# Optimization experiments

Measured on AMD Instinct MI355X. Metric: run time of the kernel, lower is better.

Reference implementation:

```python
import jax, jax.numpy as jnp
import numpy as np

GAMMA = 1.0
MAX_SIMILARITY = 1.0


def setup_inputs() -> dict:
    key = jax.random.key(0)
    k1, k2 = jax.random.split(key)
    B, Ns, D = 128, 512, 256
    d_vectors = jax.random.normal(k1, (B, Ns, D), dtype=jnp.float32)
    # Normalized similarity matrix (MinMaxScaler output lies in [0, 1])
    S = jax.random.uniform(k2, (Ns, Ns), dtype=jnp.float32)
    return {"d_vectors": d_vectors, "S": S}


def reference(d_vectors, S):
    B, Ns, D = d_vectors.shape
    eye = jnp.eye(Ns, dtype=d_vectors.dtype)

    # Pairwise squared distances: ||di||^2 + ||dj||^2 - 2 di.dj  -> [B, Ns, Ns]
    n2 = jnp.sum(d_vectors * d_vectors, axis=-1)  # [B, Ns]
    sq = n2[:, :, None] + n2[:, None, :] - 2.0 * jnp.einsum("bid,bjd->bij", d_vectors, d_vectors)
    sq = jnp.maximum(sq, 0.0) * (1.0 - eye)  # exact zero on the diagonal

    # Safe sqrt (subgradient 0 at zero distance, matching torch.norm)
    dist = jnp.where(sq > 0, jnp.sqrt(jnp.where(sq > 0, sq, 1.0)), 0.0)
    Kd = jnp.exp(-GAMMA * dist)  # Gaussian-kernel Gram matrix [B, Ns, Ns]

    # Norm-ratio loss
    W = (S > 0).astype(d_vectors.dtype)  # [Ns, Ns]
    denom = jnp.linalg.norm(W - eye)  # Frobenius norm, scalar
    Kd_tilde = Kd * (1.0 - eye)  # zero diagonal
    S_tilde = S - MAX_SIMILARITY * eye
    diff = W * (Kd_tilde - S_tilde)  # broadcast over batch
    numer = jnp.sqrt(jnp.sum(diff * diff, axis=(1, 2)))  # [B]
    losses = 2.0 * numer / denom
    return jnp.sum(losses)
```

## Files before the change

kernel.cpp:

```cpp
#include <hip/hip_runtime.h>
#include <hip/hip_bf16.h>

typedef __bf16 bf16_t;
typedef __bf16 bf16x4 __attribute__((ext_vector_type(4)));
typedef __bf16 bf16x8 __attribute__((ext_vector_type(8)));
typedef float f32x4 __attribute__((ext_vector_type(4)));
typedef float f32x16 __attribute__((ext_vector_type(16)));
typedef long i64x2 __attribute__((ext_vector_type(2)));
typedef int i32x4 __attribute__((ext_vector_type(4)));

#define BATCH 128
#define NS 512
#define DIM 256
#define BT 128
#define NT 10
#define LDSP 272

__global__ __launch_bounds__(256) void prep_st_kernel(const float* __restrict__ dv,
                                                      const float* __restrict__ S,
                                                      unsigned char* __restrict__ f8,
                                                      float* __restrict__ n2g,
                                                      float* __restrict__ St,
                                                      float* __restrict__ dpartial) {
    const int bidx = blockIdx.x;
    const int t = threadIdx.x;
    if (bidx < 256) {
        const int bi = bidx >> 4, bj = bidx & 15;
        const int c  = t & 31, r0 = t >> 5;
        __shared__ float tileS[32][33];
        __shared__ float red[4];
        float dacc = 0.0f;
#pragma unroll
        for (int k = 0; k < 4; ++k) {
            const int r  = r0 + k * 8;
            const int gi = bi * 32 + r, gj = bj * 32 + c;
            const float s = S[(size_t)gi * NS + gj];
            tileS[r][c] = s;
            const float w = (s > 0.0f) ? 1.0f : 0.0f;
            const float e = (gi == gj) ? 1.0f : 0.0f;
            const float d = w - e;
            dacc += d * d;
        }
        __syncthreads();
#pragma unroll
        for (int k = 0; k < 4; ++k) {
            const int r = r0 + k * 8;
            St[(size_t)(bj * 32 + r) * NS + bi * 32 + c] = tileS[c][r];
        }
        const int lane = t & 63, wave = t >> 6;
#pragma unroll
        for (int off = 32; off >= 1; off >>= 1) dacc += __shfl_down(dacc, off, 64);
        if (lane == 0) red[wave] = dacc;
        __syncthreads();
        if (t == 0) dpartial[bidx] = red[0] + red[1] + red[2] + red[3];
    } else {
        const int wid  = ((bidx - 256) << 2) | (t >> 6);
        const int lane = t & 63;
#pragma unroll
        for (int it = 0; it < 8; ++it) {
            const int row = wid + it * 8192;
            const f32x4 v = *reinterpret_cast<const f32x4*>(dv + (size_t)row * DIM + lane * 4);
            float pn = v[0]*v[0] + v[1]*v[1] + v[2]*v[2] + v[3]*v[3];
#pragma unroll
            for (int off = 32; off >= 1; off >>= 1) pn += __shfl_xor(pn, off, 64);
            int w0 = __builtin_amdgcn_cvt_pk_fp8_f32(v[0], v[1], 0, false);
            w0     = __builtin_amdgcn_cvt_pk_fp8_f32(v[2], v[3], w0, true);
            *reinterpret_cast<int*>(f8 + (size_t)row * DIM + lane * 4) = w0;
            if (lane == 0) n2g[row] = pn;
        }
    }
}

__global__ __launch_bounds__(512, 4) void gram_pair_kernel(const unsigned char* __restrict__ f8,
                                                           const float* __restrict__ n2g,
                                                           const float* __restrict__ S,
                                                           const float* __restrict__ St,
                                                           float* __restrict__ partial) {
    const int bid  = blockIdx.x;
    const int work = (bid & 7) * 160 + (bid >> 3);
    const int b    = work / NT;
    const int idx  = work - b * NT;
    int ti, tj;
    if (idx < 4)      { ti = 0; tj = idx; }
    else if (idx < 7) { ti = 1; tj = idx - 3; }
    else if (idx < 9) { ti = 2; tj = idx - 5; }
    else              { ti = 3; tj = 3; }
    const bool diag = (ti == tj);
    const int t    = threadIdx.x;
    const int wave = t >> 6, lane = t & 63;
    const int wr   = wave >> 2, wc = wave & 3;
    const int col  = lane & 31, kh = lane >> 5;

    __shared__ char  sP[256 * LDSP];
    __shared__ float n2s[256];
    __shared__ float red[8];

    {
        const int g     = t >> 8;
        const int tg    = t & 255;
        const int off16 = (tg & 15) * 16;
        const int rbase = tg >> 4;
        if (g == 0 || !diag) {
            const int psel = g ? tj : ti;
            const unsigned char* src = f8 + ((size_t)b * NS + (size_t)psel * BT) * DIM;
#pragma unroll
            for (int it = 0; it < 8; ++it) {
                const int row = it * 16 + rbase;
                const i32x4 v = *reinterpret_cast<const i32x4*>(src + (size_t)row * DIM + off16);
                *reinterpret_cast<i32x4*>(&sP[(g * 128 + row) * LDSP + off16]) = v;
            }
        }
        if (t < 256) {
            const int p = t >> 7;
            if (p == 0 || !diag) {
                const int psel2 = p ? tj : ti;
                n2s[t] = n2g[(size_t)b * NS + (size_t)psel2 * BT + (t & 127)];
            }
        }
    }
    __syncthreads();

    const int boff = diag ? 0 : 128;
    const char* aP = &sP[(wr * 64 + col) * LDSP + kh * 16];
    const char* bP = &sP[(boff + wc * 32 + col) * LDSP + kh * 16];
    f32x16 acc0 = (f32x16)(0.0f);
    f32x16 acc1 = (f32x16)(0.0f);
    __builtin_amdgcn_s_setprio(1);
#pragma unroll
    for (int u = 0; u < 8; ++u) {
        const i64x2 A0 = *reinterpret_cast<const i64x2*>(aP + u * 32);
        const i64x2 A1 = *reinterpret_cast<const i64x2*>(aP + 32 * LDSP + u * 32);
        const i64x2 Bv = *reinterpret_cast<const i64x2*>(bP + u * 32);
        acc0 = __builtin_amdgcn_mfma_f32_32x32x16_fp8_fp8(A0[0], Bv[0], acc0, 0, 0, 0);
        acc1 = __builtin_amdgcn_mfma_f32_32x32x16_fp8_fp8(A1[0], Bv[0], acc1, 0, 0, 0);
        acc0 = __builtin_amdgcn_mfma_f32_32x32x16_fp8_fp8(A0[1], Bv[1], acc0, 0, 0, 0);
        acc1 = __builtin_amdgcn_mfma_f32_32x32x16_fp8_fp8(A1[1], Bv[1], acc1, 0, 0, 0);
    }
    __builtin_amdgcn_s_setprio(0);

    float local = 0.0f;
    {
        const int lj = wc * 32 + col;
        const int gj = tj * BT + lj;
        const float n2j = n2s[boff + lj];
        const float* Strow = St + (size_t)gj * NS + ti * BT;
        const float* Srow  = S  + (size_t)gj * NS + ti * BT;
#pragma unroll
        for (int m = 0; m < 2; ++m) {
            const f32x16 av = m ? acc1 : acc0;
#pragma unroll
            for (int h4 = 0; h4 < 4; ++h4) {
                const int li0 = wr * 64 + m * 32 + h4 * 8 + kh * 4;
                const f32x4 s1v = *reinterpret_cast<const f32x4*>(Strow + li0);
                f32x4 s2v = (f32x4)(0.0f);
                if (!diag) s2v = *reinterpret_cast<const f32x4*>(Srow + li0);
#pragma unroll
                for (int e = 0; e < 4; ++e) {
                    const int li = li0 + e;
                    const float c = av[h4 * 4 + e];
                    const float sq = fmaxf(n2s[li] + n2j - 2.0f * c, 0.0f);
                    const float dist = __builtin_amdgcn_sqrtf(sq);
                    const float kd = __expf(-dist);
                    const float s1 = s1v[e];
                    if (diag) {
                        float d = (li == lj) ? (1.0f - s1) : (kd - s1);
                        d *= (s1 > 0.0f) ? 1.0f : 0.0f;
                        local += d * d;
                    } else {
                        const float s2 = s2v[e];
                        const float d1 = (s1 > 0.0f) ? (kd - s1) : 0.0f;
                        const float d2 = (s2 > 0.0f) ? (kd - s2) : 0.0f;
                        local += d1 * d1 + d2 * d2;
                    }
                }
            }
        }
    }

#pragma unroll
    for (int off = 32; off >= 1; off >>= 1) local += __shfl_down(local, off, 64);
    if (lane == 0) red[wave] = local;
    __syncthreads();
    if (t == 0) {
        float s = 0.0f;
#pragma unroll
        for (int w = 0; w < 8; ++w) s += red[w];
        partial[(size_t)b * NT + idx] = s;
    }
}


__global__ __launch_bounds__(256) void norms_kernel(const float* __restrict__ dv,
                                                    float* __restrict__ n2) {
    const int row  = blockIdx.x * 4 + (threadIdx.x >> 6);
    const int lane = threadIdx.x & 63;
    const float4 v = *reinterpret_cast<const float4*>(dv + (size_t)row * DIM + lane * 4);
    float s = v.x * v.x + v.y * v.y + v.z * v.z + v.w * v.w;
#pragma unroll
    for (int off = 32; off >= 1; off >>= 1) s += __shfl_down(s, off, 64);
    if (lane == 0) n2[row] = s;
}

__global__ __launch_bounds__(256) void denom_kernel(const float* __restrict__ Smat,
                                                    float* __restrict__ dpartial) {
    const int t = threadIdx.x;
    const int lane = t & 63, wave = t >> 6;
    __shared__ float sred[4];
    float acc = 0.0f;
    const int base = blockIdx.x * 512;
#pragma unroll
    for (int r = 0; r < 2; ++r) {
        const int v4 = base + r * 256 + t;
        const float4 s4 = reinterpret_cast<const float4*>(Smat)[v4];
        const int idx0 = v4 * 4;
        const int i = idx0 >> 9;
#pragma unroll
        for (int c = 0; c < 4; ++c) {
            const float s = (&s4.x)[c];
            const int j = (idx0 + c) & (NS - 1);
            const float w = (s > 0.0f) ? 1.0f : 0.0f;
            const float e = (i == j) ? 1.0f : 0.0f;
            const float d = w - e;
            acc += d * d;
        }
    }
#pragma unroll
    for (int off = 32; off >= 1; off >>= 1) acc += __shfl_down(acc, off, 64);
    if (lane == 0) sred[wave] = acc;
    __syncthreads();
    if (t == 0) dpartial[blockIdx.x] = sred[0] + sred[1] + sred[2] + sred[3];
}

#define FLDSK 40
__global__ __launch_bounds__(256) void gram_f32_kernel(const float* __restrict__ dv,
                                                       const float* __restrict__ Smat,
                                                       const float* __restrict__ n2,
                                                       float* __restrict__ partial) {
    const int tile = blockIdx.x;
    const int b    = blockIdx.y;
    const int ti   = tile >> 2, tj = tile & 3;
    const int t    = threadIdx.x;
    const int wave = t >> 6, lane = t & 63;
    const int wr   = wave >> 1, wc = wave & 1;

    __shared__ bf16_t sA[BT * FLDSK];
    __shared__ bf16_t sB[BT * FLDSK];
    __shared__ float red[4];

    const float* Abase = dv + ((size_t)b * NS + (size_t)ti * BT) * DIM;
    const float* Bbase = dv + ((size_t)b * NS + (size_t)tj * BT) * DIM;

    f32x4 acc[4][4];
#pragma unroll
    for (int m = 0; m < 4; ++m)
#pragma unroll
        for (int n = 0; n < 4; ++n) acc[m][n] = (f32x4)(0.0f);

    const int fr = lane & 15;
    const int g  = lane >> 4;

    for (int ks = 0; ks < DIM; ks += 32) {
        float4 ra[4], rb[4];
#pragma unroll
        for (int i = 0; i < 4; ++i) {
            const int c   = i * 256 + t;
            const int row = c >> 3;
            const int kc  = (c & 7) * 4;
            ra[i] = *reinterpret_cast<const float4*>(Abase + (size_t)row * DIM + ks + kc);
            rb[i] = *reinterpret_cast<const float4*>(Bbase + (size_t)row * DIM + ks + kc);
        }
        __syncthreads();
#pragma unroll
        for (int i = 0; i < 4; ++i) {
            const int c   = i * 256 + t;
            const int row = c >> 3;
            const int kc  = (c & 7) * 4;
            bf16x4 va = { (bf16_t)ra[i].x, (bf16_t)ra[i].y, (bf16_t)ra[i].z, (bf16_t)ra[i].w };
            bf16x4 vb = { (bf16_t)rb[i].x, (bf16_t)rb[i].y, (bf16_t)rb[i].z, (bf16_t)rb[i].w };
            *reinterpret_cast<bf16x4*>(&sA[row * FLDSK + kc]) = va;
            *reinterpret_cast<bf16x4*>(&sB[row * FLDSK + kc]) = vb;
        }
        __syncthreads();

        bf16x8 afrag[4], bfrag[4];
#pragma unroll
        for (int m = 0; m < 4; ++m)
            afrag[m] = *reinterpret_cast<const bf16x8*>(&sA[(wr * 64 + m * 16 + fr) * FLDSK + g * 8]);
#pragma unroll
        for (int n = 0; n < 4; ++n)
            bfrag[n] = *reinterpret_cast<const bf16x8*>(&sB[(wc * 64 + n * 16 + fr) * FLDSK + g * 8]);
#pragma unroll
        for (int m = 0; m < 4; ++m)
#pragma unroll
            for (int n = 0; n < 4; ++n)
                acc[m][n] = __builtin_amdgcn_mfma_f32_16x16x32_bf16(afrag[m], bfrag[n], acc[m][n], 0, 0, 0);
    }

    float local = 0.0f;
    const float* n2b = n2 + (size_t)b * NS;
    const int rowbase = ti * BT + wr * 64;
    const int colbase = tj * BT + wc * 64;
#pragma unroll
    for (int m = 0; m < 4; ++m) {
#pragma unroll
        for (int n = 0; n < 4; ++n) {
            const int gi0 = rowbase + m * 16 + g * 4;
            const int gj  = colbase + n * 16 + fr;
            const float ncol = n2b[gj];
#pragma unroll
            for (int j = 0; j < 4; ++j) {
                const int gi = gi0 + j;
                const float cij = acc[m][n][j];
                float sq = fmaxf(n2b[gi] + ncol - 2.0f * cij, 0.0f);
                const float dist = sqrtf(sq);
                const float kd = __expf(-dist);
                const float s = Smat[(size_t)gi * NS + gj];
                const float w = (s > 0.0f) ? 1.0f : 0.0f;
                float d = (gi == gj) ? (1.0f - s) : (kd - s);
                d *= w;
                local += d * d;
            }
        }
    }
#pragma unroll
    for (int off = 32; off >= 1; off >>= 1) local += __shfl_down(local, off, 64);
    if (lane == 0) red[wave] = local;
    __syncthreads();
    if (t == 0) partial[(size_t)b * 16 + tile] = red[0] + red[1] + red[2] + red[3];
}

__global__ __launch_bounds__(256) void finalize_kernel(const float* __restrict__ dpartial, int ndp,
                                                       const float* __restrict__ partial, int ntiles,
                                                       float* __restrict__ out) {
    const int t = threadIdx.x;
    const int lane = t & 63, wave = t >> 6;
    __shared__ float sred[4];
    __shared__ float sred2[4];

    float dacc = (t < ndp) ? dpartial[t] : 0.0f;
#pragma unroll
    for (int off = 32; off >= 1; off >>= 1) dacc += __shfl_down(dacc, off, 64);
    if (lane == 0) sred[wave] = dacc;
    __syncthreads();
    const float denom = sqrtf(sred[0] + sred[1] + sred[2] + sred[3]);

    float lsum = 0.0f;
    if (t < BATCH) {
        float ss = 0.0f;
        for (int k = 0; k < ntiles; ++k) ss += partial[(size_t)t * ntiles + k];
        lsum = 2.0f * sqrtf(ss) / denom;
    }
#pragma unroll
    for (int off = 32; off >= 1; off >>= 1) lsum += __shfl_down(lsum, off, 64);
    if (lane == 0) sred2[wave] = lsum;
    __syncthreads();
    if (t == 0) out[0] = sred2[0] + sred2[1] + sred2[2] + sred2[3];
}

extern "C" void kernel_launch(void* const* d_in, const int* in_sizes, int n_in,
                              void* d_out, int out_size, void* d_ws, size_t ws_size,
                              hipStream_t stream) {
    const float* dv   = (const float*)d_in[0];
    const float* Smat = (const float*)d_in[1];
    float* out = (float*)d_out;

    const size_t f8_bytes = (size_t)BATCH * NS * DIM;
    const size_t st_bytes = (size_t)NS * NS * 4;
    const size_t n2_bytes = (size_t)BATCH * NS * 4;
    const size_t pt_bytes = (size_t)BATCH * 16 * 4;
    const size_t dp_bytes = 256 * 4;
    const size_t need = f8_bytes + st_bytes + n2_bytes + pt_bytes + dp_bytes;

    if (ws_size >= need) {
        char* w = (char*)d_ws;
        unsigned char* f8 = (unsigned char*)w;  w += f8_bytes;
        float* St      = (float*)w;   w += st_bytes;
        float* n2g     = (float*)w;   w += n2_bytes;
        float* partial = (float*)w;   w += pt_bytes;
        float* dpart   = (float*)w;

        prep_st_kernel<<<dim3(2304), 256, 0, stream>>>(dv, Smat, f8, n2g, St, dpart);
        gram_pair_kernel<<<dim3(NT * BATCH), 512, 0, stream>>>(f8, n2g, Smat, St, partial);
        finalize_kernel<<<dim3(1), 256, 0, stream>>>(dpart, 256, partial, NT, out);
    } else {
        float* n2      = (float*)d_ws;
        float* partial = n2 + (size_t)BATCH * NS;
        float* dpart   = partial + (size_t)BATCH * 16;

        norms_kernel<<<dim3(BATCH * NS / 4), 256, 0, stream>>>(dv, n2);
        denom_kernel<<<dim3(128), 256, 0, stream>>>(Smat, dpart);
        gram_f32_kernel<<<dim3(16, BATCH), 256, 0, stream>>>(dv, Smat, n2, partial);
        finalize_kernel<<<dim3(1), 256, 0, stream>>>(dpart, 128, partial, 16, out);
    }
}
```

Baseline: 51.90 us.

## Stage Gram kernel values in LDS to read S rows coalesced

The epilogue now writes exp(-dist) for the tile into shared memory, reusing the operand buffer, then re-reads it in a row-major thread mapping. This lets each thread load S and its transpose as contiguous float4 along rows instead of column-strided reads of the transposed copy. It adds two block barriers and an LDS round trip per tile, and the loads now come from S for the first term and St for the second, swapping their roles.

Measured after the change: 45.48 us. -12.4%, faster.

```diff
diff --git a/kernel.cpp b/kernel.cpp
--- a/kernel.cpp
+++ b/kernel.cpp
@@ -15,6 +15,7 @@
 #define BT 128
 #define NT 10
 #define LDSP 272
+#define CSTRIDE 132
 
 __global__ __launch_bounds__(256) void prep_st_kernel(const float* __restrict__ dv,
                                                       const float* __restrict__ S,
@@ -91,9 +92,11 @@
     const int wr   = wave >> 2, wc = wave & 3;
     const int col  = lane & 31, kh = lane >> 5;
 
-    __shared__ char  sP[256 * LDSP];
+    __shared__ __attribute__((aligned(16))) char smem[256 * LDSP];
     __shared__ float n2s[256];
     __shared__ float red[8];
+    char*  sP = smem;
+    float* sC = reinterpret_cast<float*>(smem);
 
     {
         const int g     = t >> 8;
@@ -137,41 +140,61 @@
         acc1 = __builtin_amdgcn_mfma_f32_32x32x16_fp8_fp8(A1[1], Bv[1], acc1, 0, 0, 0);
     }
     __builtin_amdgcn_s_setprio(0);
+    __syncthreads();
+
+    {
+        const int lj = wc * 32 + col;
+        const float n2j = n2s[boff + lj];
+#pragma unroll
+        for (int m = 0; m < 2; ++m) {
+            const f32x16 av = m ? acc1 : acc0;
+#pragma unroll
+            for (int h4 = 0; h4 < 4; ++h4) {
+#pragma unroll
+                for (int e = 0; e < 4; ++e) {
+                    const int li = wr * 64 + m * 32 + h4 * 8 + kh * 4 + e;
+                    const float c = av[h4 * 4 + e];
+                    const float sq = fmaxf(n2s[li] + n2j - 2.0f * c, 0.0f);
+                    sC[li * CSTRIDE + lj] = __expf(-__builtin_amdgcn_sqrtf(sq));
+                }
+            }
+        }
+    }
+    __syncthreads();
 
     float local = 0.0f;
     {
-        const int lj = wc * 32 + col;
-        const int gj = tj * BT + lj;
-        const float n2j = n2s[boff + lj];
-        const float* Strow = St + (size_t)gj * NS + ti * BT;
-        const float* Srow  = S  + (size_t)gj * NS + ti * BT;
-#pragma unroll
-        for (int m = 0; m < 2; ++m) {
-            const f32x16 av = m ? acc1 : acc0;
-#pragma unroll
-            for (int h4 = 0; h4 < 4; ++h4) {
-                const int li0 = wr * 64 + m * 32 + h4 * 8 + kh * 4;
-                const f32x4 s1v = *reinterpret_cast<const f32x4*>(Strow + li0);
-                f32x4 s2v = (f32x4)(0.0f);
-                if (!diag) s2v = *reinterpret_cast<const f32x4*>(Srow + li0);
-#pragma unroll
-                for (int e = 0; e < 4; ++e) {
-                    const int li = li0 + e;
-                    const float c = av[h4 * 4 + e];
-                    const float sq = fmaxf(n2s[li] + n2j - 2.0f * c, 0.0f);
-                    const float dist = __builtin_amdgcn_sqrtf(sq);
-                    const float kd = __expf(-dist);
-                    const float s1 = s1v[e];
-                    if (diag) {
-                        float d = (li == lj) ? (1.0f - s1) : (kd - s1);
-                        d *= (s1 > 0.0f) ? 1.0f : 0.0f;
-                        local += d * d;
-                    } else {
-                        const float s2 = s2v[e];
-                        const float d1 = (s1 > 0.0f) ? (kd - s1) : 0.0f;
-                        const float d2 = (s2 > 0.0f) ? (kd - s2) : 0.0f;
-                        local += d1 * d1 + d2 * d2;
-                    }
+        const int rg = t >> 4;
+        const int ln = t & 15;
+        f32x4 s1a[8], s2a[8];
+#pragma unroll
+        for (int it = 0; it < 8; ++it) {
+            const int li  = rg + (it >> 1) * 32;
+            const int ljb = (it & 1) * 64 + ln * 4;
+            const int gi  = ti * BT + li;
+            s1a[it] = *reinterpret_cast<const f32x4*>(S  + (size_t)gi * NS + tj * BT + ljb);
+            s2a[it] = diag ? (f32x4)(0.0f)
+                           : *reinterpret_cast<const f32x4*>(St + (size_t)gi * NS + tj * BT + ljb);
+        }
+#pragma unroll
+        for (int it = 0; it < 8; ++it) {
+            const int li  = rg + (it >> 1) * 32;
+            const int ljb = (it & 1) * 64 + ln * 4;
+            const f32x4 kdv = *reinterpret_cast<const f32x4*>(&sC[li * CSTRIDE + ljb]);
+#pragma unroll
+            for (int e = 0; e < 4; ++e) {
+                const int lj = ljb + e;
+                const float kd = kdv[e];
+                const float s1 = s1a[it][e];
+                if (diag) {
+                    float d = (li == lj) ? (1.0f - s1) : (kd - s1);
+                    d *= (s1 > 0.0f) ? 1.0f : 0.0f;
+                    local += d * d;
+                } else {
+                    const float s2 = s2a[it][e];
+                    const float d1 = (s1 > 0.0f) ? (kd - s1) : 0.0f;
+                    const float d2 = (s2 > 0.0f) ? (kd - s2) : 0.0f;
+                    local += d1 * d1 + d2 * d2;
                 }
             }
         }
```
